# Optimization experiments

Measured on AMD Instinct MI355X. Metric: run time of the kernel, lower is better.

## Reference

```python
import jax, jax.numpy as jnp
import numpy as np

# Per-species MLP dims from CoefficientLayer._create_model (H, C, N, O), aev_dim=384
DIMS = {"h": [384, 160, 128, 96, 1], "c": [384, 144, 112, 96, 1], "n": [384, 128, 112, 96, 1], "o": [384, 128, 112, 96, 1]}


def setup_inputs() -> dict:
    key = jax.random.key(0)
    B, A, D = 256, 256, 384
    ks = jax.random.split(key, 64)
    inp = {}
    inp["species"] = jax.random.randint(ks[0], (B, A), 0, 4)  # species index 0..3
    inp["aev"] = jax.random.normal(ks[1], (B, A, D), dtype=jnp.float32)
    inp["b0"] = jnp.array([0.1, 0.2, 0.3, 0.4], dtype=jnp.float32)  # shifter intercepts
    inp["b1"] = jnp.array([1.0, 1.1, 0.9, 1.2], dtype=jnp.float32)  # shifter slopes
    ki = 2
    for name, dims in DIMS.items():
        for l in range(4):
            fi, fo = dims[l], dims[l + 1]
            inp[f"{name}w{l}"] = jax.random.normal(ks[ki], (fi, fo), dtype=jnp.float32) / np.float32(np.sqrt(fi))
            ki += 1
            inp[f"{name}b{l}"] = jnp.zeros((fo,), dtype=jnp.float32)
    return inp


def _mlp(x, ws, bs):
    # Linear -> CELU(0.1) x3 -> Linear(->1), squeeze last dim
    for i in range(3):
        x = jax.nn.celu(x @ ws[i] + bs[i], alpha=0.1)
    return (x @ ws[3] + bs[3])[..., 0]


def reference(species, aev, b0, b1,
              hw0, hb0, hw1, hb1, hw2, hb2, hw3, hb3,
              cw0, cb0, cw1, cb1, cw2, cb2, cw3, cb3,
              nw0, nb0, nw1, nb1, nw2, nb2, nw3, nb3,
              ow0, ob0, ow1, ob1, ow2, ob2, ow3, ob3):
    nets = [
        ([hw0, hw1, hw2, hw3], [hb0, hb1, hb2, hb3]),
        ([cw0, cw1, cw2, cw3], [cb0, cb1, cb2, cb3]),
        ([nw0, nw1, nw2, nw3], [nb0, nb1, nb2, nb3]),
        ([ow0, ow1, ow2, ow3], [ob0, ob1, ob2, ob3]),
    ]
    # ANIModel hard routing: each atom's coefficient comes from its species' network;
    # atoms with species == -1 (padding) stay 0.
    coef = jnp.zeros(species.shape, dtype=aev.dtype)
    for i, (ws, bs) in enumerate(nets):  # fixed small loop over 4 species
        coef = jnp.where(species == i, _mlp(aev, ws, bs), coef)
    # Shifter: result[mask_i] = b0[i] + b1[i] * coef[mask_i]; padding stays 0
    idx = jnp.clip(species, 0)
    return jnp.where(species >= 0, b0[idx] + b1[idx] * coef, jnp.zeros((), dtype=aev.dtype))
```

## Files before the change

### kernel.cpp

```cpp
#include <hip/hip_runtime.h>

typedef _Float16 f16;
typedef _Float16 f16x8 __attribute__((ext_vector_type(8)));
typedef float f32x4 __attribute__((ext_vector_type(4)));
typedef unsigned short u16;

#define NATOMS 65536
#define SLOT 5120
#define RING 3

#define WS_LISTS_OFF 256
#define WS_W_OFF 524544
#define WS_W_ELEMS 350208
#define WS_NEEDED (WS_W_OFF + WS_W_ELEMS * 2)

struct ConvJob { const float* src; int K, N, KS, NT, CK, off; };

struct PrepParams {
  const int* species;
  int* counts;
  u16* lists;
  f16* wbase;
  ConvJob jobs[16];
};

struct MlpParams {
  const float* aev;
  const float* b0;
  const float* b1;
  const float* bias[4][4];
  const f16* w[4][4];
  const int* counts;
  const u16* lists;
  float* out;
  int Nreal0[4];
  int Nreal1[4];
};

template <int N> struct AF { f16x8 v[N]; };

__global__ __launch_bounds__(256) void prep_kernel(PrepParams p) {
  int tid = threadIdx.x;
  if (blockIdx.x < 256) {
    __shared__ int wcnt[4][4];
    __shared__ int wbase[4][4];
    int i = blockIdx.x * 256 + tid;
    int s = p.species[i];
    int wave = tid >> 6, lane = tid & 63;
    unsigned long long m[4];
    #pragma unroll
    for (int t = 0; t < 4; t++) {
      m[t] = __ballot(s == t);
      if (lane == 0) wcnt[wave][t] = __popcll(m[t]);
    }
    __syncthreads();
    if (tid < 4) {
      int t = tid;
      int c0 = wcnt[0][t], c1 = wcnt[1][t], c2 = wcnt[2][t], c3 = wcnt[3][t];
      int base = atomicAdd(&p.counts[t], c0 + c1 + c2 + c3);
      wbase[0][t] = base;
      wbase[1][t] = base + c0;
      wbase[2][t] = base + c0 + c1;
      wbase[3][t] = base + c0 + c1 + c2;
    }
    __syncthreads();
    int rnk = __popcll(m[s] & ((1ull << lane) - 1ull));
    p.lists[s * NATOMS + wbase[wave][s] + rnk] = (u16)i;
  } else {
    int bx = blockIdx.x - 256;
    int job = bx / 30, bxin = bx - job * 30;
    ConvJob jb = p.jobs[job];
    int e = bxin * 256 + tid;
    int nslots = jb.KS * jb.NT * 64;
    if (e >= nslots) return;
    int frag = e >> 6, lane = e & 63;
    int c = frag / (jb.CK * jb.NT);
    int rem = frag - c * (jb.CK * jb.NT);
    int ckc = min(jb.CK, jb.KS - c * jb.CK);
    int nt = rem / ckc, ki = rem - nt * ckc;
    int ks = c * jb.CK + ki;
    int q = lane >> 4, nlo = lane & 15;
    int n = nt * 16 + nlo;
    int k0 = ks * 32 + q * 8;
    f16x8 v;
    #pragma unroll
    for (int j = 0; j < 8; j++) {
      int k = k0 + j;
      float x = (n < jb.N && k < jb.K) ? jb.src[k * jb.N + n] : 0.f;
      v[j] = (f16)x;
    }
    *(f16x8*)(p.wbase + jb.off + (size_t)e * 8) = v;
  }
}

__device__ __forceinline__ float celu01(float v) {
  return v > 0.f ? v : 0.1f * (__expf(v * 10.f) - 1.f);
}

__device__ __forceinline__ void stage_frag(const f16* g, f16* l, int lane) {
  __builtin_amdgcn_global_load_lds(
      (const __attribute__((address_space(1))) unsigned int*)(g + lane * 8),
      (__attribute__((address_space(3))) unsigned int*)l, 16, 0, 0);
}

template <int NT0, int KS1>
struct Sched {
  static constexpr int NC = 12 + KS1 + 4 + 1;
  static constexpr int frags(int c) {
    return c < 12 ? NT0 : (c < 12 + KS1 ? 8 : (c < 12 + KS1 + 4 ? 6 : 3));
  }
};

template <int NT0, int KS1, int C>
__device__ __forceinline__ void issue_chunk(const f16* w0, const f16* w1,
                                            const f16* w2, const f16* w3,
                                            f16* ring, int lane) {
  constexpr int NF = Sched<NT0, KS1>::frags(C);
  const f16* g;
  if constexpr (C < 12) g = w0 + (size_t)C * NT0 * 512;
  else if constexpr (C < 12 + KS1) g = w1 + (size_t)(C - 12) * 8 * 512;
  else if constexpr (C < 12 + KS1 + 4) g = w2 + (size_t)(C - 12 - KS1) * 6 * 512;
  else g = w3;
  f16* l = ring + (C % RING) * SLOT;
  #pragma unroll
  for (int f = 0; f < NF; f++)
    stage_frag(g + f * 512, l + f * 512, lane);
}

template <int NT0, int KS1, int C>
__device__ void prod_step(const f16* w0, const f16* w1, const f16* w2, const f16* w3,
                          f16* ring, volatile int* flag, volatile int* done, int lane) {
  constexpr int NC = Sched<NT0, KS1>::NC;
  constexpr int NXT = (C + 1 < NC) ? Sched<NT0, KS1>::frags(C + 1) : 0;
  __builtin_amdgcn_s_waitcnt((NXT & 15) | ((NXT >> 4) << 14) | 0x0F70);
  if (lane == 0) flag[C] = 1;
  if constexpr (C + 2 < NC) {
    if constexpr (C >= 1) {
      while (done[C - 1] < 4) __builtin_amdgcn_s_sleep(1);
    }
    issue_chunk<NT0, KS1, C + 2>(w0, w1, w2, w3, ring, lane);
  }
  if constexpr (C + 1 < NC)
    prod_step<NT0, KS1, C + 1>(w0, w1, w2, w3, ring, flag, done, lane);
}

template <int KS, int NT, int CB, bool ACT>
__device__ __forceinline__ void consume_layer(AF<KS> a, const f16* ring,
                                              int* flag, int* done,
                                              const float* __restrict__ bias, int Nreal,
                                              f16* dstw, int lane, int q, int nlo) {
  f32x4 acc[NT];
  #pragma unroll
  for (int nt = 0; nt < NT; nt++) acc[nt] = f32x4{0.f, 0.f, 0.f, 0.f};
  #pragma unroll
  for (int c = 0; c < KS; c++) {
    while (__hip_atomic_load(&flag[CB + c], __ATOMIC_ACQUIRE,
                             __HIP_MEMORY_SCOPE_WORKGROUP) == 0)
      __builtin_amdgcn_s_sleep(1);
    const f16* slot = ring + ((CB + c) % RING) * SLOT;
    #pragma unroll
    for (int nt = 0; nt < NT; nt++) {
      f16x8 b = *(const f16x8*)(slot + nt * 512 + lane * 8);
      acc[nt] = __builtin_amdgcn_mfma_f32_16x16x32_f16(a.v[c], b, acc[nt], 0, 0, 0);
    }
    if (lane == 0)
      __hip_atomic_fetch_add(&done[CB + c], 1, __ATOMIC_RELEASE,
                             __HIP_MEMORY_SCOPE_WORKGROUP);
  }
  #pragma unroll
  for (int nt = 0; nt < NT; nt++) {
    int n = nt * 16 + nlo;
    float bv = (n < Nreal) ? bias[n] : 0.f;
    #pragma unroll
    for (int r = 0; r < 4; r++) {
      float v = acc[nt][r] + bv;
      if (ACT) v = celu01(v);
      dstw[(q * 4 + r) * 168 + n] = (f16)v;
    }
  }
}

template <int NT0, int KS1>
__device__ __forceinline__ void mlp_body(const MlpParams& p, int s, int tile,
                                         f16* ring, f16* Bf, int* flag, int* done) {
  int cnt = p.counts[s];
  if (tile * 64 >= cnt) return;
  int tid = threadIdx.x, w = tid >> 6, lane = tid & 63;
  if (tid < 24) flag[tid] = 0;
  else if (tid < 48) done[tid - 24] = 0;
  __syncthreads();

  if (w == 4) {
    const f16 *w0 = p.w[s][0], *w1 = p.w[s][1], *w2 = p.w[s][2], *w3 = p.w[s][3];
    issue_chunk<NT0, KS1, 0>(w0, w1, w2, w3, ring, lane);
    issue_chunk<NT0, KS1, 1>(w0, w1, w2, w3, ring, lane);
    prod_step<NT0, KS1, 0>(w0, w1, w2, w3, ring, (volatile int*)flag,
                           (volatile int*)done, lane);
    return;
  }

  const u16* list = p.lists + s * NATOMS;
  int q = lane >> 4, nlo = lane & 15;
  int rowbase = tile * 64 + w * 16;
  int atom = list[min(rowbase + nlo, cnt - 1)];

  AF<12> a0;
  const float* ap = p.aev + (size_t)atom * 384 + q * 8;
  #pragma unroll
  for (int ks = 0; ks < 12; ks++) {
    float4 u0 = *(const float4*)(ap + ks * 32);
    float4 u1 = *(const float4*)(ap + ks * 32 + 4);
    f16x8 t = {(f16)u0.x, (f16)u0.y, (f16)u0.z, (f16)u0.w,
               (f16)u1.x, (f16)u1.y, (f16)u1.z, (f16)u1.w};
    a0.v[ks] = t;
  }

  f16* my = Bf + (w * 16) * 168;

  consume_layer<12, NT0, 0, true>(a0, ring, flag, done, p.bias[s][0], p.Nreal0[s],
                                  my, lane, q, nlo);
  AF<KS1> a1;
  #pragma unroll
  for (int ks = 0; ks < KS1; ks++)
    a1.v[ks] = *(const f16x8*)(my + nlo * 168 + ks * 32 + q * 8);
  consume_layer<KS1, 8, 12, true>(a1, ring, flag, done, p.bias[s][1], p.Nreal1[s],
                                  my, lane, q, nlo);
  AF<4> a2;
  #pragma unroll
  for (int ks = 0; ks < 4; ks++)
    a2.v[ks] = *(const f16x8*)(my + nlo * 168 + ks * 32 + q * 8);
  consume_layer<4, 6, 12 + KS1, true>(a2, ring, flag, done, p.bias[s][2], 96,
                                      my, lane, q, nlo);

  AF<3> a3;
  #pragma unroll
  for (int ks = 0; ks < 3; ks++)
    a3.v[ks] = *(const f16x8*)(my + nlo * 168 + ks * 32 + q * 8);
  constexpr int G3 = 12 + KS1 + 4;
  while (__hip_atomic_load(&flag[G3], __ATOMIC_ACQUIRE,
                           __HIP_MEMORY_SCOPE_WORKGROUP) == 0)
    __builtin_amdgcn_s_sleep(1);
  const f16* slot = ring + (G3 % RING) * SLOT;
  f32x4 acc3 = {0.f, 0.f, 0.f, 0.f};
  #pragma unroll
  for (int ks = 0; ks < 3; ks++) {
    f16x8 b = *(const f16x8*)(slot + ks * 512 + lane * 8);
    acc3 = __builtin_amdgcn_mfma_f32_16x16x32_f16(a3.v[ks], b, acc3, 0, 0, 0);
  }
  if (nlo == 0) {
    float b3 = p.bias[s][3][0];
    float b0v = p.b0[s], b1v = p.b1[s];
    #pragma unroll
    for (int r = 0; r < 4; r++) {
      int m = rowbase + q * 4 + r;
      if (m < cnt) {
        float coef = acc3[r] + b3;
        p.out[list[m]] = b0v + b1v * coef;
      }
    }
  }
}

__global__ __launch_bounds__(320, 4) void mlp_kernel(MlpParams p) {
  __shared__ f16 ring[RING * SLOT];
  __shared__ f16 Bf[64 * 168];
  __shared__ int flag[24];
  __shared__ int done[24];
  int s = blockIdx.x & 3;
  int tile = blockIdx.x >> 2;
  switch (s) {
    case 0: mlp_body<10, 5>(p, 0, tile, ring, Bf, flag, done); break;
    case 1: mlp_body<10, 5>(p, 1, tile, ring, Bf, flag, done); break;
    case 2: mlp_body<8, 4>(p, 2, tile, ring, Bf, flag, done); break;
    default: mlp_body<8, 4>(p, 3, tile, ring, Bf, flag, done); break;
  }
}

extern "C" void kernel_launch(void* const* d_in, const int* in_sizes, int n_in,
                              void* d_out, int out_size, void* d_ws, size_t ws_size,
                              hipStream_t stream) {
  if (ws_size < WS_NEEDED) return;

  const int* species = (const int*)d_in[0];
  const float* aev = (const float*)d_in[1];
  const float* b0 = (const float*)d_in[2];
  const float* b1 = (const float*)d_in[3];

  static const int F1[4]  = {160, 144, 128, 128};
  static const int F1p[4] = {160, 160, 128, 128};
  static const int F2[4]  = {128, 112, 112, 112};

  char* wsb = (char*)d_ws;
  int* counts = (int*)wsb;
  u16* lists = (u16*)(wsb + WS_LISTS_OFF);
  f16* wbase = (f16*)(wsb + WS_W_OFF);

  PrepParams pp;
  pp.species = species; pp.counts = counts; pp.lists = lists; pp.wbase = wbase;

  MlpParams mp;
  mp.aev = aev; mp.b0 = b0; mp.b1 = b1;
  mp.counts = counts; mp.lists = lists; mp.out = (float*)d_out;

  int off = 0, ji = 0;
  for (int s = 0; s < 4; s++) {
    int K[4]  = {384, F1[s], F2[s], 96};
    int N[4]  = {F1[s], F2[s], 96, 1};
    int KS[4] = {12, F1p[s] / 32, 4, 3};
    int NT[4] = {F1p[s] / 16, 8, 6, 1};
    int CK[4] = {1, 1, 1, 3};
    for (int l = 0; l < 4; l++) {
      const float* w = (const float*)d_in[4 + s * 8 + l * 2];
      const float* b = (const float*)d_in[4 + s * 8 + l * 2 + 1];
      pp.jobs[ji].src = w;
      pp.jobs[ji].K = K[l];
      pp.jobs[ji].N = N[l];
      pp.jobs[ji].KS = KS[l];
      pp.jobs[ji].NT = NT[l];
      pp.jobs[ji].CK = CK[l];
      pp.jobs[ji].off = off;
      mp.w[s][l] = wbase + off;
      mp.bias[s][l] = b;
      off += KS[l] * NT[l] * 512;
      ji++;
    }
    mp.Nreal0[s] = F1[s];
    mp.Nreal1[s] = F2[s];
  }

  hipMemsetAsync(d_ws, 0, 64, stream);
  prep_kernel<<<dim3(256 + 480), 256, 0, stream>>>(pp);
  mlp_kernel<<<dim3(280 * 4), 320, 0, stream>>>(mp);
}
```

Baseline: 263.7 us.

## Replace producer-wave ring with barrier-synced double buffer and 128-row tiles

Drops the dedicated producer wave and its flag/done spin-wait handshake over a 3-slot LDS ring. All eight compute waves now cooperatively stage the next weight chunk into a 2-slot double buffer, with a __syncthreads after each K-chunk. Each block also grows from 64 to 128 atoms, so every staged weight chunk is reused across twice as many rows and half as many blocks are launched. The trade-off is a full block barrier per chunk, which can stall the MFMA stream, plus larger LDS and register use per block that may lower occupancy.

Measured after the change: 268.6 us. Within noise of the previous version (+1.9%).

```diff
diff --git a/kernel.cpp b/kernel.cpp
--- a/kernel.cpp
+++ b/kernel.cpp
@@ -7,7 +7,7 @@
 
 #define NATOMS 65536
 #define SLOT 5120
-#define RING 3
+#define NBUF 2
 
 #define WS_LISTS_OFF 256
 #define WS_W_OFF 524544
@@ -38,6 +38,7 @@
 };
 
 template <int N> struct AF { f16x8 v[N]; };
+template <int N> struct ACC { f32x4 v[N]; };
 
 __global__ __launch_bounds__(256) void prep_kernel(PrepParams p) {
   int tid = threadIdx.x;
@@ -112,68 +113,58 @@
 };
 
 template <int NT0, int KS1, int C>
-__device__ __forceinline__ void issue_chunk(const f16* w0, const f16* w1,
+__device__ __forceinline__ void stage_chunk(const f16* w0, const f16* w1,
                                             const f16* w2, const f16* w3,
-                                            f16* ring, int lane) {
+                                            f16* ring, int w, int lane) {
   constexpr int NF = Sched<NT0, KS1>::frags(C);
   const f16* g;
   if constexpr (C < 12) g = w0 + (size_t)C * NT0 * 512;
   else if constexpr (C < 12 + KS1) g = w1 + (size_t)(C - 12) * 8 * 512;
   else if constexpr (C < 12 + KS1 + 4) g = w2 + (size_t)(C - 12 - KS1) * 6 * 512;
   else g = w3;
-  f16* l = ring + (C % RING) * SLOT;
-  #pragma unroll
-  for (int f = 0; f < NF; f++)
-    stage_frag(g + f * 512, l + f * 512, lane);
-}
-
-template <int NT0, int KS1, int C>
-__device__ void prod_step(const f16* w0, const f16* w1, const f16* w2, const f16* w3,
-                          f16* ring, volatile int* flag, volatile int* done, int lane) {
-  constexpr int NC = Sched<NT0, KS1>::NC;
-  constexpr int NXT = (C + 1 < NC) ? Sched<NT0, KS1>::frags(C + 1) : 0;
-  __builtin_amdgcn_s_waitcnt((NXT & 15) | ((NXT >> 4) << 14) | 0x0F70);
-  if (lane == 0) flag[C] = 1;
-  if constexpr (C + 2 < NC) {
-    if constexpr (C >= 1) {
-      while (done[C - 1] < 4) __builtin_amdgcn_s_sleep(1);
-    }
-    issue_chunk<NT0, KS1, C + 2>(w0, w1, w2, w3, ring, lane);
-  }
-  if constexpr (C + 1 < NC)
-    prod_step<NT0, KS1, C + 1>(w0, w1, w2, w3, ring, flag, done, lane);
-}
-
-template <int KS, int NT, int CB, bool ACT>
-__device__ __forceinline__ void consume_layer(AF<KS> a, const f16* ring,
-                                              int* flag, int* done,
-                                              const float* __restrict__ bias, int Nreal,
-                                              f16* dstw, int lane, int q, int nlo) {
-  f32x4 acc[NT];
-  #pragma unroll
-  for (int nt = 0; nt < NT; nt++) acc[nt] = f32x4{0.f, 0.f, 0.f, 0.f};
-  #pragma unroll
-  for (int c = 0; c < KS; c++) {
-    while (__hip_atomic_load(&flag[CB + c], __ATOMIC_ACQUIRE,
-                             __HIP_MEMORY_SCOPE_WORKGROUP) == 0)
-      __builtin_amdgcn_s_sleep(1);
-    const f16* slot = ring + ((CB + c) % RING) * SLOT;
+  f16* l = ring + (C % NBUF) * SLOT;
+  if (w < NF) stage_frag(g + w * 512, l + w * 512, lane);
+  if constexpr (NF > 8) {
+    if (w + 8 < NF) stage_frag(g + (w + 8) * 512, l + (w + 8) * 512, lane);
+  }
+}
+
+template <int NT0, int KS1, int CB, int KS, int NT, int I>
+__device__ __forceinline__ ACC<NT> layer_step(AF<KS> a, ACC<NT> acc, f16* ring,
+    const f16* s0, const f16* s1, const f16* s2, const f16* s3, int w, int lane) {
+  if constexpr (I == KS) {
+    return acc;
+  } else {
+    constexpr int G = CB + I;
+    if constexpr (G + 1 < Sched<NT0, KS1>::NC)
+      stage_chunk<NT0, KS1, G + 1>(s0, s1, s2, s3, ring, w, lane);
+    const f16* slot = ring + (G % NBUF) * SLOT;
     #pragma unroll
     for (int nt = 0; nt < NT; nt++) {
       f16x8 b = *(const f16x8*)(slot + nt * 512 + lane * 8);
-      acc[nt] = __builtin_amdgcn_mfma_f32_16x16x32_f16(a.v[c], b, acc[nt], 0, 0, 0);
-    }
-    if (lane == 0)
-      __hip_atomic_fetch_add(&done[CB + c], 1, __ATOMIC_RELEASE,
-                             __HIP_MEMORY_SCOPE_WORKGROUP);
-  }
+      acc.v[nt] = __builtin_amdgcn_mfma_f32_16x16x32_f16(a.v[I], b, acc.v[nt], 0, 0, 0);
+    }
+    __syncthreads();
+    return layer_step<NT0, KS1, CB, KS, NT, I + 1>(a, acc, ring, s0, s1, s2, s3, w, lane);
+  }
+}
+
+template <int NT0, int KS1, int CB, int KS, int NT, bool ACT>
+__device__ __forceinline__ void consume_layer(AF<KS> a, f16* ring,
+    const f16* s0, const f16* s1, const f16* s2, const f16* s3,
+    const float* __restrict__ bias, int Nreal, f16* dstw, int w, int lane,
+    int q, int nlo) {
+  ACC<NT> acc;
+  #pragma unroll
+  for (int nt = 0; nt < NT; nt++) acc.v[nt] = f32x4{0.f, 0.f, 0.f, 0.f};
+  acc = layer_step<NT0, KS1, CB, KS, NT, 0>(a, acc, ring, s0, s1, s2, s3, w, lane);
   #pragma unroll
   for (int nt = 0; nt < NT; nt++) {
     int n = nt * 16 + nlo;
     float bv = (n < Nreal) ? bias[n] : 0.f;
     #pragma unroll
     for (int r = 0; r < 4; r++) {
-      float v = acc[nt][r] + bv;
+      float v = acc.v[nt][r] + bv;
       if (ACT) v = celu01(v);
       dstw[(q * 4 + r) * 168 + n] = (f16)v;
     }
@@ -182,26 +173,17 @@
 
 template <int NT0, int KS1>
 __device__ __forceinline__ void mlp_body(const MlpParams& p, int s, int tile,
-                                         f16* ring, f16* Bf, int* flag, int* done) {
+                                         f16* ring, f16* Bf) {
   int cnt = p.counts[s];
-  if (tile * 64 >= cnt) return;
+  if (tile * 128 >= cnt) return;
   int tid = threadIdx.x, w = tid >> 6, lane = tid & 63;
-  if (tid < 24) flag[tid] = 0;
-  else if (tid < 48) done[tid - 24] = 0;
-  __syncthreads();
-
-  if (w == 4) {
-    const f16 *w0 = p.w[s][0], *w1 = p.w[s][1], *w2 = p.w[s][2], *w3 = p.w[s][3];
-    issue_chunk<NT0, KS1, 0>(w0, w1, w2, w3, ring, lane);
-    issue_chunk<NT0, KS1, 1>(w0, w1, w2, w3, ring, lane);
-    prod_step<NT0, KS1, 0>(w0, w1, w2, w3, ring, (volatile int*)flag,
-                           (volatile int*)done, lane);
-    return;
-  }
+  const f16 *s0 = p.w[s][0], *s1 = p.w[s][1], *s2 = p.w[s][2], *s3 = p.w[s][3];
+
+  stage_chunk<NT0, KS1, 0>(s0, s1, s2, s3, ring, w, lane);
 
   const u16* list = p.lists + s * NATOMS;
   int q = lane >> 4, nlo = lane & 15;
-  int rowbase = tile * 64 + w * 16;
+  int rowbase = tile * 128 + w * 16;
   int atom = list[min(rowbase + nlo, cnt - 1)];
 
   AF<12> a0;
@@ -214,33 +196,31 @@
                (f16)u1.x, (f16)u1.y, (f16)u1.z, (f16)u1.w};
     a0.v[ks] = t;
   }
+  __syncthreads();
 
   f16* my = Bf + (w * 16) * 168;
 
-  consume_layer<12, NT0, 0, true>(a0, ring, flag, done, p.bias[s][0], p.Nreal0[s],
-                                  my, lane, q, nlo);
+  consume_layer<NT0, KS1, 0, 12, NT0, true>(a0, ring, s0, s1, s2, s3,
+      p.bias[s][0], p.Nreal0[s], my, w, lane, q, nlo);
   AF<KS1> a1;
   #pragma unroll
   for (int ks = 0; ks < KS1; ks++)
     a1.v[ks] = *(const f16x8*)(my + nlo * 168 + ks * 32 + q * 8);
-  consume_layer<KS1, 8, 12, true>(a1, ring, flag, done, p.bias[s][1], p.Nreal1[s],
-                                  my, lane, q, nlo);
+  consume_layer<NT0, KS1, 12, KS1, 8, true>(a1, ring, s0, s1, s2, s3,
+      p.bias[s][1], p.Nreal1[s], my, w, lane, q, nlo);
   AF<4> a2;
   #pragma unroll
   for (int ks = 0; ks < 4; ks++)
     a2.v[ks] = *(const f16x8*)(my + nlo * 168 + ks * 32 + q * 8);
-  consume_layer<4, 6, 12 + KS1, true>(a2, ring, flag, done, p.bias[s][2], 96,
-                                      my, lane, q, nlo);
+  consume_layer<NT0, KS1, 12 + KS1, 4, 6, true>(a2, ring, s0, s1, s2, s3,
+      p.bias[s][2], 96, my, w, lane, q, nlo);
 
   AF<3> a3;
   #pragma unroll
   for (int ks = 0; ks < 3; ks++)
     a3.v[ks] = *(const f16x8*)(my + nlo * 168 + ks * 32 + q * 8);
   constexpr int G3 = 12 + KS1 + 4;
-  while (__hip_atomic_load(&flag[G3], __ATOMIC_ACQUIRE,
-                           __HIP_MEMORY_SCOPE_WORKGROUP) == 0)
-    __builtin_amdgcn_s_sleep(1);
-  const f16* slot = ring + (G3 % RING) * SLOT;
+  const f16* slot = ring + (G3 % NBUF) * SLOT;
   f32x4 acc3 = {0.f, 0.f, 0.f, 0.f};
   #pragma unroll
   for (int ks = 0; ks < 3; ks++) {
@@ -261,18 +241,16 @@
   }
 }
 
-__global__ __launch_bounds__(320, 4) void mlp_kernel(MlpParams p) {
-  __shared__ f16 ring[RING * SLOT];
-  __shared__ f16 Bf[64 * 168];
-  __shared__ int flag[24];
-  __shared__ int done[24];
+__global__ __launch_bounds__(512, 4) void mlp_kernel(MlpParams p) {
+  __shared__ __align__(16) f16 ring[NBUF * SLOT];
+  __shared__ __align__(16) f16 Bf[128 * 168];
   int s = blockIdx.x & 3;
   int tile = blockIdx.x >> 2;
   switch (s) {
-    case 0: mlp_body<10, 5>(p, 0, tile, ring, Bf, flag, done); break;
-    case 1: mlp_body<10, 5>(p, 1, tile, ring, Bf, flag, done); break;
-    case 2: mlp_body<8, 4>(p, 2, tile, ring, Bf, flag, done); break;
-    default: mlp_body<8, 4>(p, 3, tile, ring, Bf, flag, done); break;
+    case 0: mlp_body<10, 5>(p, 0, tile, ring, Bf); break;
+    case 1: mlp_body<10, 5>(p, 1, tile, ring, Bf); break;
+    case 2: mlp_body<8, 4>(p, 2, tile, ring, Bf); break;
+    default: mlp_body<8, 4>(p, 3, tile, ring, Bf); break;
   }
 }
 
@@ -330,5 +308,5 @@
 
   hipMemsetAsync(d_ws, 0, 64, stream);
   prep_kernel<<<dim3(256 + 480), 256, 0, stream>>>(pp);
-  mlp_kernel<<<dim3(280 * 4), 320, 0, stream>>>(mp);
-}
+  mlp_kernel<<<dim3(140 * 4), 512, 0, stream>>>(mp);
+}
```
